# Kernel tuning notes

Measured on AMD Instinct MI355X. Metric: run time of the kernel, lower is better.

## Reference

```python
import jax, jax.numpy as jnp
import numpy as np

B, N, D_MODEL = 4, 4096, 1024
HEADS, DIM_HEAD = 16, 64
HIDDEN = HEADS * DIM_HEAD
SCALE = DIM_HEAD ** -0.5


def setup_inputs() -> dict:
    key = jax.random.key(0)
    k1, k2, k3, k4 = jax.random.split(key, 4)
    x = jax.random.normal(k1, (B, N, D_MODEL), dtype=jnp.float32)
    w_qkv = jax.random.normal(k2, (D_MODEL, 3 * HIDDEN), dtype=jnp.float32) * (D_MODEL ** -0.5)
    w_out = jax.random.normal(k3, (HIDDEN, D_MODEL), dtype=jnp.float32) * (HIDDEN ** -0.5)
    b_out = jax.random.normal(k4, (D_MODEL,), dtype=jnp.float32) * 0.01
    return {"x": x, "w_qkv": w_qkv, "w_out": w_out, "b_out": b_out}


def reference(x, w_qkv, w_out, b_out):
    b, n, _ = x.shape
    qkv = x @ w_qkv  # [b, n, 3*hidden]
    q, k, v = jnp.split(qkv, 3, axis=-1)

    def to_bhdn(t):
        # 'b n (h d) -> b h d n'
        return t.reshape(b, n, HEADS, DIM_HEAD).transpose(0, 2, 3, 1)

    q, k, v = map(to_bhdn, (q, k, v))
    q = jax.nn.softmax(q, axis=-2) * SCALE  # softmax over feature dim d
    k = jax.nn.softmax(k, axis=-1)          # softmax over sequence dim n
    context = jnp.einsum('bhdn,bhen->bhde', k, v)  # [b,h,d,e], d=e=dim_head
    out = jnp.einsum('bhde,bhdn->bhen', context, q)
    # 'b h e n -> b n (h e)'
    out = out.transpose(0, 3, 1, 2).reshape(b, n, HIDDEN)
    return out @ w_out + b_out
```

## Files before the change

kernel.cpp:

```cpp
#include <hip/hip_runtime.h>
#include <hip/hip_bf16.h>


typedef unsigned short u16t;
typedef __bf16 bf16x8 __attribute__((ext_vector_type(8)));
typedef float f32x4 __attribute__((ext_vector_type(4)));
typedef unsigned short ushort8 __attribute__((ext_vector_type(8)));

__device__ __forceinline__ u16t f2bf(float f) {
    union { float f; unsigned int u; } v; v.f = f;
    unsigned int r = v.u + 0x7fffu + ((v.u >> 16) & 1u);
    return (u16t)(r >> 16);
}
__device__ __forceinline__ float bf2f(u16t h) {
    union { unsigned int u; float f; } v; v.u = ((unsigned int)h) << 16;
    return v.f;
}

#define GLOAD_LDS16(gptr, lptr) \
    __builtin_amdgcn_global_load_lds((const __attribute__((address_space(1))) unsigned int*)(gptr), \
                                     (__attribute__((address_space(3))) unsigned int*)(lptr), 16, 0, 0)
#define SFENCE asm volatile("" ::: "memory")

__global__ __launch_bounds__(256) void prep_kernel(const float* __restrict__ x, u16t* __restrict__ xb,
                                                   const float* __restrict__ w_qkv, u16t* __restrict__ wqkvT,
                                                   const float* __restrict__ w_out, u16t* __restrict__ woutT,
                                                   float* __restrict__ zbase) {
    int bid = blockIdx.x, t = threadIdx.x;
    if (bid < 2048) {
        int i = (bid * 256 + t) * 4;
        for (; i < 16777216; i += 2048 * 256 * 4) {
            float4 v = *(const float4*)(x + i);
            ushort4 o;
            o.x = f2bf(v.x); o.y = f2bf(v.y); o.z = f2bf(v.z); o.w = f2bf(v.w);
            *(ushort4*)(xb + i) = o;
        }
        return;
    }
    if (bid >= 6144) {
        float4* z = (float4*)zbase;
        int i = (bid - 6144) * 256 + t;
        for (; i < 69632; i += 68 * 256) z[i] = make_float4(0.f, 0.f, 0.f, 0.f);
        return;
    }
    __shared__ float tile[32][33];
    const float* in; u16t* out; int R, C, bx, by;
    if (bid < 5120) { in = w_qkv; out = wqkvT; R = 1024; C = 3072; int b2 = bid - 2048; bx = b2 % 96; by = b2 / 96; }
    else            { in = w_out; out = woutT; R = 1024; C = 1024; int b3 = bid - 5120; bx = b3 & 31; by = b3 >> 5; }
    int c0 = bx * 32, r0 = by * 32;
    int tx = t & 31, ty = t >> 5;
    for (int i = 0; i < 32; i += 8)
        tile[ty + i][tx] = in[(size_t)(r0 + ty + i) * C + c0 + tx];
    __syncthreads();
    for (int i = 0; i < 32; i += 8)
        out[(size_t)(c0 + ty + i) * R + r0 + tx] = f2bf(tile[tx][ty + i]);
}

template<int OUTF32, int BIAS, int BATCHB, int KSUM>
__device__ __forceinline__ void gemm256_body(const u16t* __restrict__ A, const u16t* __restrict__ Bt,
                                             void* __restrict__ Cout, const float* __restrict__ bias,
                                             float* __restrict__ ksum,
                                             int M, int N, int K, int NBX, int lda) {
    __shared__ __align__(16) u16t lds[65536];
    const int t = threadIdx.x;
    const int l = t & 63, w = t >> 6;
    const int wm = w >> 2, wn = w & 3;

    int cpx = gridDim.x >> 3;
    int wg = ((int)blockIdx.x & 7) * cpx + ((int)blockIdx.x >> 3);
    int bx = wg % NBX, by = wg / NBX;
    const int m0 = by * 256, n0 = bx * 256;
    const int NT = K >> 6;
    if (BATCHB) Bt += (size_t)(by >> 4) << 20;

    const int colk0 = ((l >> 4) ^ (l & 7)) * 8;
    const int colk1 = colk0 ^ 32;
    const int abase = (wm * 32 + (l & 15)) * 64;
    const int bbase = 16384 + (wn >> 1) * 8192 + ((wn & 1) * 64 + (l & 15)) * 64;

    const int rr = w * 8 + (l >> 3);
    const int coloff = ((l ^ (l >> 3)) & 7) * 8;
    const int rowA = rr + ((rr >= 32) ? 96 : 0);
    const u16t* pa_st = A  + (size_t)(m0 + rowA) * lda + coloff;
    const u16t* pb_st = Bt + (size_t)(n0 + rr) * K + coloff;
    const int so = w * 512;

#define SPAIR(qq, kto, pb) do { \
    size_t k64_ = (size_t)(kto) * 64; \
    if ((qq) == 0) { \
        GLOAD_LDS16(pb_st + k64_,                  &lds[(pb) * 32768 + 16384 + so]); \
        GLOAD_LDS16(pb_st + k64_ + (size_t)64 * K, &lds[(pb) * 32768 + 20480 + so]); \
    } else if ((qq) == 1) { \
        GLOAD_LDS16(pb_st + k64_ + (size_t)128 * K, &lds[(pb) * 32768 + 24576 + so]); \
        GLOAD_LDS16(pb_st + k64_ + (size_t)192 * K, &lds[(pb) * 32768 + 28672 + so]); \
    } else if ((qq) == 2) { \
        GLOAD_LDS16(pa_st + k64_,                    &lds[(pb) * 32768 + so]); \
        GLOAD_LDS16(pa_st + k64_ + (size_t)32 * lda, &lds[(pb) * 32768 + 4096 + so]); \
    } else { \
        GLOAD_LDS16(pa_st + k64_ + (size_t)64 * lda, &lds[(pb) * 32768 + 8192 + so]); \
        GLOAD_LDS16(pa_st + k64_ + (size_t)96 * lda, &lds[(pb) * 32768 + 12288 + so]); \
    } \
} while (0)

    f32x4 acc[8][4] = {};

    SPAIR(0, 0, 0); SPAIR(1, 0, 0); SPAIR(2, 0, 0);
    SFENCE;
    SPAIR(3, 0, 0);

    for (int kt = 0; kt < NT; ++kt) {
        const int p = kt & 1;
        const bool sn = (kt + 1 < NT);
        const u16t* lA = &lds[p * 32768];

        asm volatile("s_waitcnt vmcnt(2)" ::: "memory");
        __builtin_amdgcn_s_barrier();

        bf16x8 bfr[4][2];
#pragma unroll
        for (int ni = 0; ni < 4; ++ni) {
            bfr[ni][0] = *(const bf16x8*)&lA[bbase + ni * 1024 + colk0];
            bfr[ni][1] = *(const bf16x8*)&lA[bbase + ni * 1024 + colk1];
        }
        bf16x8 af1[2][2][2];
#pragma unroll
        for (int g = 0; g < 2; ++g) {
            af1[g][0][0] = *(const bf16x8*)&lA[g * 4096 + abase + colk0];
            af1[g][0][1] = *(const bf16x8*)&lA[g * 4096 + abase + colk1];
            af1[g][1][0] = *(const bf16x8*)&lA[g * 4096 + abase + 1024 + colk0];
            af1[g][1][1] = *(const bf16x8*)&lA[g * 4096 + abase + 1024 + colk1];
        }
        if (sn) { SPAIR(0, kt + 1, p ^ 1); SPAIR(1, kt + 1, p ^ 1); SPAIR(2, kt + 1, p ^ 1); }
        __builtin_amdgcn_s_setprio(1);
#pragma unroll
        for (int g = 0; g < 2; ++g)
#pragma unroll
            for (int dm = 0; dm < 2; ++dm)
#pragma unroll
                for (int ni = 0; ni < 4; ++ni)
#pragma unroll
                    for (int kk = 0; kk < 2; ++kk)
                        acc[g * 2 + dm][ni] = __builtin_amdgcn_mfma_f32_16x16x32_bf16(
                            af1[g][dm][kk], bfr[ni][kk], acc[g * 2 + dm][ni], 0, 0, 0);
        __builtin_amdgcn_s_setprio(0);

        if (sn) asm volatile("s_waitcnt vmcnt(6)" ::: "memory");
        else    asm volatile("s_waitcnt vmcnt(0)" ::: "memory");
        __builtin_amdgcn_s_barrier();

        bf16x8 af2[2][2][2];
#pragma unroll
        for (int g = 0; g < 2; ++g) {
            af2[g][0][0] = *(const bf16x8*)&lA[(g + 2) * 4096 + abase + colk0];
            af2[g][0][1] = *(const bf16x8*)&lA[(g + 2) * 4096 + abase + colk1];
            af2[g][1][0] = *(const bf16x8*)&lA[(g + 2) * 4096 + abase + 1024 + colk0];
            af2[g][1][1] = *(const bf16x8*)&lA[(g + 2) * 4096 + abase + 1024 + colk1];
        }
        if (sn) SPAIR(3, kt + 1, p ^ 1);
        __builtin_amdgcn_s_setprio(1);
#pragma unroll
        for (int g = 0; g < 2; ++g)
#pragma unroll
            for (int dm = 0; dm < 2; ++dm)
#pragma unroll
                for (int ni = 0; ni < 4; ++ni)
#pragma unroll
                    for (int kk = 0; kk < 2; ++kk)
                        acc[4 + g * 2 + dm][ni] = __builtin_amdgcn_mfma_f32_16x16x32_bf16(
                            af2[g][dm][kk], bfr[ni][kk], acc[4 + g * 2 + dm][ni], 0, 0, 0);
        __builtin_amdgcn_s_setprio(0);
    }
#undef SPAIR

    if (KSUM && n0 >= 1024 && n0 < 2048) {
#pragma unroll
        for (int ni = 0; ni < 4; ++ni) {
            int col = n0 + wn * 64 + ni * 16 + (l & 15);
            float se = 0.f;
#pragma unroll
            for (int mi = 0; mi < 8; ++mi) {
                int row = m0 + wm * 128 + mi * 16 + ((l >> 4) << 2);
#pragma unroll
                for (int j = 0; j < 4; ++j) {
                    float e = __expf(acc[mi][ni][j]);
                    se += e;
                    ((u16t*)Cout)[(size_t)(row + j) * N + col] = f2bf(e);
                }
            }
            se += __shfl_xor(se, 16);
            se += __shfl_xor(se, 32);
            if ((l >> 4) == 0)
                atomicAdd(&ksum[(by >> 4) * 1024 + (n0 - 1024) + wn * 64 + ni * 16 + l], se);
        }
    } else {
#pragma unroll
        for (int mi = 0; mi < 8; ++mi) {
            int row = m0 + wm * 128 + mi * 16 + ((l >> 4) << 2);
#pragma unroll
            for (int ni = 0; ni < 4; ++ni) {
                int col = n0 + wn * 64 + ni * 16 + (l & 15);
                float bv = BIAS ? bias[col] : 0.f;
#pragma unroll
                for (int j = 0; j < 4; ++j) {
                    float v = acc[mi][ni][j] + bv;
                    if (OUTF32) ((float*)Cout)[(size_t)(row + j) * N + col] = v;
                    else        ((u16t*)Cout)[(size_t)(row + j) * N + col] = f2bf(v);
                }
            }
        }
    }
}

__global__ __launch_bounds__(512, 2) void gemm_qkv(const u16t* __restrict__ A, const u16t* __restrict__ Bt,
                                                   u16t* __restrict__ C, float* __restrict__ ksum) {
    gemm256_body<0, 0, 0, 1>(A, Bt, C, nullptr, ksum, 16384, 3072, 1024, 12, 1024);
}

__global__ __launch_bounds__(512, 2) void gemm_out(const u16t* __restrict__ A, const u16t* __restrict__ Bt,
                                                   float* __restrict__ C, const float* __restrict__ bias) {
    gemm256_body<1, 1, 1, 0>(A, Bt, C, bias, nullptr, 16384, 1024, 1024, 4, 3072);
}

__global__ __launch_bounds__(256) void post_qkv(u16t* __restrict__ qkv,
                                                const float* __restrict__ ksum,
                                                float* __restrict__ ctxT) {
    int bid = blockIdx.x, t = threadIdx.x;
    if (bid < 512) {
        int bh = bid >> 3, chunk = bid & 7;
        int b = bh >> 4, h = bh & 15;
        __shared__ u16t kT[64 * 136];
        __shared__ u16t vT[64 * 136];
        int lane = t & 63, w = t >> 6;
        f32x4 acc[4] = {};
        for (int sub = 0; sub < 4; sub++) {
            size_t rowbase = ((size_t)b * 4096 + chunk * 512 + sub * 128) * 3072 + h * 64;
#pragma unroll
            for (int i = 0; i < 4; i++) {
                int P = t + 256 * i;
                int n = P >> 3, c = P & 7;
                size_t ro = rowbase + (size_t)n * 3072 + c * 8;
                ushort8 k8 = *(const ushort8*)(&qkv[ro + 1024]);
                ushort8 v8 = *(const ushort8*)(&qkv[ro + 2048]);
                int nx = n ^ (c << 3);
#pragma unroll
                for (int j = 0; j < 8; j++) {
                    kT[(c * 8 + j) * 136 + nx] = k8[j];
                    vT[(c * 8 + j) * 136 + nx] = v8[j];
                }
            }
            __syncthreads();
#pragma unroll
            for (int ks = 0; ks < 4; ks++) {
                int er = w * 16 + (lane & 15);
                int nb = ks * 32 + ((lane >> 4) << 3);
                bf16x8 a = *(const bf16x8*)(&vT[er * 136 + (nb ^ ((er >> 3) << 3))]);
#pragma unroll
                for (int ct = 0; ct < 4; ct++) {
                    int dr = ct * 16 + (lane & 15);
                    bf16x8 bb = *(const bf16x8*)(&kT[dr * 136 + (nb ^ ((dr >> 3) << 3))]);
                    acc[ct] = __builtin_amdgcn_mfma_f32_16x16x32_bf16(a, bb, acc[ct], 0, 0, 0);
                }
            }
            __syncthreads();
        }
#pragma unroll
        for (int ct = 0; ct < 4; ct++) {
            int e = w * 16 + ((lane >> 4) << 2);
            int dd = ct * 16 + (lane & 15);
            float gi = 1.0f / ksum[b * 1024 + h * 64 + dd];
#pragma unroll
            for (int j = 0; j < 4; j++)
                atomicAdd(&ctxT[(size_t)bh * 4096 + (e + j) * 64 + dd], acc[ct][j] * gi);
        }
        return;
    }
    int qb = bid - 512;
#pragma unroll
    for (int it = 0; it < 8; ++it) {
        int r = qb * 256 + it * 32 + (t >> 3);
        size_t addr = (size_t)(r >> 4) * 3072 + (r & 15) * 64 + (t & 7) * 8;
        ushort8 ch = *(const ushort8*)(&qkv[addr]);
        float v0 = bf2f(ch[0]), v1 = bf2f(ch[1]), v2 = bf2f(ch[2]), v3 = bf2f(ch[3]);
        float v4 = bf2f(ch[4]), v5 = bf2f(ch[5]), v6 = bf2f(ch[6]), v7 = bf2f(ch[7]);
        float m = fmaxf(fmaxf(fmaxf(v0, v1), fmaxf(v2, v3)), fmaxf(fmaxf(v4, v5), fmaxf(v6, v7)));
        m = fmaxf(m, __shfl_xor(m, 1)); m = fmaxf(m, __shfl_xor(m, 2)); m = fmaxf(m, __shfl_xor(m, 4));
        float e0 = __expf(v0 - m), e1 = __expf(v1 - m), e2 = __expf(v2 - m), e3 = __expf(v3 - m);
        float e4 = __expf(v4 - m), e5 = __expf(v5 - m), e6 = __expf(v6 - m), e7 = __expf(v7 - m);
        float s = e0 + e1 + e2 + e3 + e4 + e5 + e6 + e7;
        s += __shfl_xor(s, 1); s += __shfl_xor(s, 2); s += __shfl_xor(s, 4);
        float inv = 0.125f / s;
        ushort8 o;
        o[0] = f2bf(e0 * inv); o[1] = f2bf(e1 * inv); o[2] = f2bf(e2 * inv); o[3] = f2bf(e3 * inv);
        o[4] = f2bf(e4 * inv); o[5] = f2bf(e5 * inv); o[6] = f2bf(e6 * inv); o[7] = f2bf(e7 * inv);
        *(ushort8*)(&qkv[addr]) = o;
    }
}

__global__ __launch_bounds__(256) void w2_kernel(const float* __restrict__ ctxT,
                                                 const u16t* __restrict__ woutT,
                                                 u16t* __restrict__ w2t) {
    int bh = blockIdx.x, jc = blockIdx.y;
    int b = bh >> 4, h = bh & 15;
    __shared__ u16t cb[64][72];
    __shared__ u16t wl[256][72];
    int t = threadIdx.x;
#pragma unroll
    for (int i = 0; i < 16; i++) {
        int f = t + 256 * i;
        cb[f & 63][f >> 6] = f2bf(ctxT[(size_t)bh * 4096 + f]);
    }
#pragma unroll
    for (int i = 0; i < 8; i++) {
        int f = t + 256 * i;
        int r = f >> 3, q = f & 7;
        *(uint4*)(&wl[r][q * 8]) = *(const uint4*)(&woutT[(size_t)(jc * 256 + r) * 1024 + h * 64 + q * 8]);
    }
    __syncthreads();
    int l = t & 63, w = t >> 6;
    f32x4 acc[4][4] = {};
#pragma unroll
    for (int kk = 0; kk < 2; kk++) {
        bf16x8 af[4], bfr[4];
#pragma unroll
        for (int mt = 0; mt < 4; mt++)
            af[mt] = *(const bf16x8*)&wl[w * 64 + mt * 16 + (l & 15)][(l >> 4) * 8 + kk * 32];
#pragma unroll
        for (int nt = 0; nt < 4; nt++)
            bfr[nt] = *(const bf16x8*)&cb[nt * 16 + (l & 15)][(l >> 4) * 8 + kk * 32];
#pragma unroll
        for (int mt = 0; mt < 4; mt++)
#pragma unroll
            for (int nt = 0; nt < 4; nt++)
                acc[mt][nt] = __builtin_amdgcn_mfma_f32_16x16x32_bf16(af[mt], bfr[nt], acc[mt][nt], 0, 0, 0);
    }
#pragma unroll
    for (int mt = 0; mt < 4; mt++) {
        int j = jc * 256 + w * 64 + mt * 16 + ((l >> 4) << 2);
#pragma unroll
        for (int nt = 0; nt < 4; nt++) {
            int dd = nt * 16 + (l & 15);
#pragma unroll
            for (int jj = 0; jj < 4; jj++)
                w2t[((size_t)b << 20) + (size_t)(j + jj) * 1024 + h * 64 + dd] = f2bf(acc[mt][nt][jj]);
        }
    }
}


extern "C" void kernel_launch(void* const* d_in, const int* in_sizes, int n_in,
                              void* d_out, int out_size, void* d_ws, size_t ws_size,
                              hipStream_t stream) {
    const float* x     = (const float*)d_in[0];
    const float* w_qkv = (const float*)d_in[1];
    const float* w_out = (const float*)d_in[2];
    const float* b_out = (const float*)d_in[3];
    float* out = (float*)d_out;
    char* ws = (char*)d_ws;

    size_t o_xb    = 0;
    size_t o_wqkvT = 33554432;
    size_t o_woutT = 39845888;
    size_t o_qkv   = 41943040;
    size_t o_ctx   = 142606336;
    size_t o_ksum  = 143654912;
    size_t needed  = 143720448;
    if (ws_size < needed) return;

    u16t* xb     = (u16t*)(ws + o_xb);
    u16t* w2t    = (u16t*)(ws + o_xb);
    u16t* wqkvT  = (u16t*)(ws + o_wqkvT);
    u16t* woutT  = (u16t*)(ws + o_woutT);
    u16t* qkvb   = (u16t*)(ws + o_qkv);
    float* ctxT  = (float*)(ws + o_ctx);
    float* ksum  = (float*)(ws + o_ksum);

    prep_kernel<<<6212, 256, 0, stream>>>(x, xb, w_qkv, wqkvT, w_out, woutT, ctxT);

    gemm_qkv<<<768, 512, 0, stream>>>(xb, wqkvT, qkvb, ksum);

    post_qkv<<<1536, 256, 0, stream>>>(qkvb, ksum, ctxT);

    w2_kernel<<<dim3(64, 4), 256, 0, stream>>>(ctxT, woutT, w2t);

    gemm_out<<<256, 512, 0, stream>>>(qkvb, w2t, out, b_out);
}
```

Before: 193.8 us.

## Fuse K-softmax exp and KᵀV context into QKV GEMM epilogue, drop K/V round trip

The QKV GEMM now pairs the K and V columns of a head pair in each output tile. Its epilogue computes exp(K), stages exp(K) and V transposed in LDS, runs a small MFMA KᵀV, and atomically accumulates the context, so K and V are never written to or re-read from global memory. The K-softmax normalisation (1/ksum) moves into w2_kernel, and the Q feature softmax becomes a standalone kernel. The cost is extra LDS work and synchronisation in the GEMM epilogue, plus many more atomics on ctxT, one per 256-row tile instead of per 512-row chunk.

```diff
diff --git a/kernel.cpp b/kernel.cpp
--- a/kernel.cpp
+++ b/kernel.cpp
@@ -6,6 +6,7 @@
 typedef __bf16 bf16x8 __attribute__((ext_vector_type(8)));
 typedef float f32x4 __attribute__((ext_vector_type(4)));
 typedef unsigned short ushort8 __attribute__((ext_vector_type(8)));
+typedef unsigned short u16x4 __attribute__((ext_vector_type(4)));
 
 __device__ __forceinline__ u16t f2bf(float f) {
     union { float f; unsigned int u; } v; v.f = f;
@@ -56,10 +57,10 @@
         out[(size_t)(c0 + ty + i) * R + r0 + tx] = f2bf(tile[tx][ty + i]);
 }
 
-template<int OUTF32, int BIAS, int BATCHB, int KSUM>
+template<int OUTF32, int BIAS, int BATCHB, int KV>
 __device__ __forceinline__ void gemm256_body(const u16t* __restrict__ A, const u16t* __restrict__ Bt,
                                              void* __restrict__ Cout, const float* __restrict__ bias,
-                                             float* __restrict__ ksum,
+                                             float* __restrict__ ksum, float* __restrict__ ctxT,
                                              int M, int N, int K, int NBX, int lda) {
     __shared__ __align__(16) u16t lds[65536];
     const int t = threadIdx.x;
@@ -81,18 +82,22 @@
     const int rr = w * 8 + (l >> 3);
     const int coloff = ((l ^ (l >> 3)) & 7) * 8;
     const int rowA = rr + ((rr >= 32) ? 96 : 0);
-    const u16t* pa_st = A  + (size_t)(m0 + rowA) * lda + coloff;
-    const u16t* pb_st = Bt + (size_t)(n0 + rr) * K + coloff;
+    const u16t* pa_st = A + (size_t)(m0 + rowA) * lda + coloff;
+    int rb0, rb1;
+    if (KV && bx >= 4) { int hp = bx - 4; rb0 = 1024 + hp * 128; rb1 = 2048 + hp * 128; }
+    else               { rb0 = n0; rb1 = n0 + 128; }
+    const u16t* pb0 = Bt + (size_t)(rb0 + rr) * K + coloff;
+    const u16t* pb1 = Bt + (size_t)(rb1 + rr) * K + coloff;
     const int so = w * 512;
 
 #define SPAIR(qq, kto, pb) do { \
     size_t k64_ = (size_t)(kto) * 64; \
     if ((qq) == 0) { \
-        GLOAD_LDS16(pb_st + k64_,                  &lds[(pb) * 32768 + 16384 + so]); \
-        GLOAD_LDS16(pb_st + k64_ + (size_t)64 * K, &lds[(pb) * 32768 + 20480 + so]); \
+        GLOAD_LDS16(pb0 + k64_,                  &lds[(pb) * 32768 + 16384 + so]); \
+        GLOAD_LDS16(pb0 + k64_ + (size_t)64 * K, &lds[(pb) * 32768 + 20480 + so]); \
     } else if ((qq) == 1) { \
-        GLOAD_LDS16(pb_st + k64_ + (size_t)128 * K, &lds[(pb) * 32768 + 24576 + so]); \
-        GLOAD_LDS16(pb_st + k64_ + (size_t)192 * K, &lds[(pb) * 32768 + 28672 + so]); \
+        GLOAD_LDS16(pb1 + k64_,                  &lds[(pb) * 32768 + 24576 + so]); \
+        GLOAD_LDS16(pb1 + k64_ + (size_t)64 * K, &lds[(pb) * 32768 + 28672 + so]); \
     } else if ((qq) == 2) { \
         GLOAD_LDS16(pa_st + k64_,                    &lds[(pb) * 32768 + so]); \
         GLOAD_LDS16(pa_st + k64_ + (size_t)32 * lda, &lds[(pb) * 32768 + 4096 + so]); \
@@ -172,25 +177,75 @@
     }
 #undef SPAIR
 
-    if (KSUM && n0 >= 1024 && n0 < 2048) {
-#pragma unroll
-        for (int ni = 0; ni < 4; ++ni) {
-            int col = n0 + wn * 64 + ni * 16 + (l & 15);
-            float se = 0.f;
-#pragma unroll
-            for (int mi = 0; mi < 8; ++mi) {
-                int row = m0 + wm * 128 + mi * 16 + ((l >> 4) << 2);
-#pragma unroll
-                for (int j = 0; j < 4; ++j) {
-                    float e = __expf(acc[mi][ni][j]);
-                    se += e;
-                    ((u16t*)Cout)[(size_t)(row + j) * N + col] = f2bf(e);
+    if (KV && bx >= 4) {
+        const int hp = bx - 4;
+        const int bb = by >> 4;
+        __syncthreads();
+        u16t* ekT = lds;
+        u16t* vT  = lds + 32768;
+#define EADDR(dp, r) ((dp) * 256 + ((r) ^ (((dp) & 15) << 2)))
+        if (wn < 2) {
+#pragma unroll
+            for (int ni = 0; ni < 4; ++ni) {
+                int dp = wn * 64 + ni * 16 + (l & 15);
+                float se = 0.f;
+#pragma unroll
+                for (int mi = 0; mi < 8; ++mi) {
+                    int r0 = wm * 128 + mi * 16 + ((l >> 4) << 2);
+                    u16x4 pk;
+#pragma unroll
+                    for (int j = 0; j < 4; ++j) { float e = __expf(acc[mi][ni][j]); se += e; pk[j] = f2bf(e); }
+                    *(u16x4*)&ekT[EADDR(dp, r0)] = pk;
+                }
+                se += __shfl_xor(se, 16);
+                se += __shfl_xor(se, 32);
+                if ((l >> 4) == 0)
+                    atomicAdd(&ksum[bb * 1024 + hp * 128 + dp], se);
+            }
+        } else {
+#pragma unroll
+            for (int ni = 0; ni < 4; ++ni) {
+                int ep = (wn - 2) * 64 + ni * 16 + (l & 15);
+#pragma unroll
+                for (int mi = 0; mi < 8; ++mi) {
+                    int r0 = wm * 128 + mi * 16 + ((l >> 4) << 2);
+                    u16x4 pv;
+#pragma unroll
+                    for (int j = 0; j < 4; ++j) pv[j] = f2bf(acc[mi][ni][j]);
+                    *(u16x4*)&vT[EADDR(ep, r0)] = pv;
                 }
             }
-            se += __shfl_xor(se, 16);
-            se += __shfl_xor(se, 32);
-            if ((l >> 4) == 0)
-                atomicAdd(&ksum[(by >> 4) * 1024 + (n0 - 1024) + wn * 64 + ni * 16 + l], se);
+        }
+        __syncthreads();
+        const int head = w >> 2, tn = w & 3;
+        const int dp2 = head * 64 + tn * 16 + (l & 15);
+        const int sb2 = (dp2 & 15) << 2;
+        f32x4 acc2[4] = {};
+#pragma unroll
+        for (int ks = 0; ks < 8; ++ks) {
+            int rk = ks * 32 + ((l >> 4) << 3);
+            union { u16x4 h[2]; bf16x8 v; } bu;
+            bu.h[0] = *(const u16x4*)&ekT[dp2 * 256 + (rk ^ sb2)];
+            bu.h[1] = *(const u16x4*)&ekT[dp2 * 256 + ((rk + 4) ^ sb2)];
+#pragma unroll
+            for (int tm = 0; tm < 4; ++tm) {
+                int ep = head * 64 + tm * 16 + (l & 15);
+                int sa = (ep & 15) << 2;
+                union { u16x4 h[2]; bf16x8 v; } au;
+                au.h[0] = *(const u16x4*)&vT[ep * 256 + (rk ^ sa)];
+                au.h[1] = *(const u16x4*)&vT[ep * 256 + ((rk + 4) ^ sa)];
+                acc2[tm] = __builtin_amdgcn_mfma_f32_16x16x32_bf16(au.v, bu.v, acc2[tm], 0, 0, 0);
+            }
+        }
+#undef EADDR
+        int bh = bb * 16 + hp * 2 + head;
+#pragma unroll
+        for (int tm = 0; tm < 4; ++tm) {
+            int e = tm * 16 + ((l >> 4) << 2);
+            int dd = tn * 16 + (l & 15);
+#pragma unroll
+            for (int j = 0; j < 4; ++j)
+                atomicAdd(&ctxT[(size_t)bh * 4096 + (e + j) * 64 + dd], acc2[tm][j]);
         }
     } else {
 #pragma unroll
@@ -212,72 +267,21 @@
 }
 
 __global__ __launch_bounds__(512, 2) void gemm_qkv(const u16t* __restrict__ A, const u16t* __restrict__ Bt,
-                                                   u16t* __restrict__ C, float* __restrict__ ksum) {
-    gemm256_body<0, 0, 0, 1>(A, Bt, C, nullptr, ksum, 16384, 3072, 1024, 12, 1024);
+                                                   u16t* __restrict__ C, float* __restrict__ ksum,
+                                                   float* __restrict__ ctxT) {
+    gemm256_body<0, 0, 0, 1>(A, Bt, C, nullptr, ksum, ctxT, 16384, 3072, 1024, 12, 1024);
 }
 
 __global__ __launch_bounds__(512, 2) void gemm_out(const u16t* __restrict__ A, const u16t* __restrict__ Bt,
                                                    float* __restrict__ C, const float* __restrict__ bias) {
-    gemm256_body<1, 1, 1, 0>(A, Bt, C, bias, nullptr, 16384, 1024, 1024, 4, 3072);
-}
-
-__global__ __launch_bounds__(256) void post_qkv(u16t* __restrict__ qkv,
-                                                const float* __restrict__ ksum,
-                                                float* __restrict__ ctxT) {
-    int bid = blockIdx.x, t = threadIdx.x;
-    if (bid < 512) {
-        int bh = bid >> 3, chunk = bid & 7;
-        int b = bh >> 4, h = bh & 15;
-        __shared__ u16t kT[64 * 136];
-        __shared__ u16t vT[64 * 136];
-        int lane = t & 63, w = t >> 6;
-        f32x4 acc[4] = {};
-        for (int sub = 0; sub < 4; sub++) {
-            size_t rowbase = ((size_t)b * 4096 + chunk * 512 + sub * 128) * 3072 + h * 64;
-#pragma unroll
-            for (int i = 0; i < 4; i++) {
-                int P = t + 256 * i;
-                int n = P >> 3, c = P & 7;
-                size_t ro = rowbase + (size_t)n * 3072 + c * 8;
-                ushort8 k8 = *(const ushort8*)(&qkv[ro + 1024]);
-                ushort8 v8 = *(const ushort8*)(&qkv[ro + 2048]);
-                int nx = n ^ (c << 3);
-#pragma unroll
-                for (int j = 0; j < 8; j++) {
-                    kT[(c * 8 + j) * 136 + nx] = k8[j];
-                    vT[(c * 8 + j) * 136 + nx] = v8[j];
-                }
-            }
-            __syncthreads();
-#pragma unroll
-            for (int ks = 0; ks < 4; ks++) {
-                int er = w * 16 + (lane & 15);
-                int nb = ks * 32 + ((lane >> 4) << 3);
-                bf16x8 a = *(const bf16x8*)(&vT[er * 136 + (nb ^ ((er >> 3) << 3))]);
-#pragma unroll
-                for (int ct = 0; ct < 4; ct++) {
-                    int dr = ct * 16 + (lane & 15);
-                    bf16x8 bb = *(const bf16x8*)(&kT[dr * 136 + (nb ^ ((dr >> 3) << 3))]);
-                    acc[ct] = __builtin_amdgcn_mfma_f32_16x16x32_bf16(a, bb, acc[ct], 0, 0, 0);
-                }
-            }
-            __syncthreads();
-        }
-#pragma unroll
-        for (int ct = 0; ct < 4; ct++) {
-            int e = w * 16 + ((lane >> 4) << 2);
-            int dd = ct * 16 + (lane & 15);
-            float gi = 1.0f / ksum[b * 1024 + h * 64 + dd];
-#pragma unroll
-            for (int j = 0; j < 4; j++)
-                atomicAdd(&ctxT[(size_t)bh * 4096 + (e + j) * 64 + dd], acc[ct][j] * gi);
-        }
-        return;
-    }
-    int qb = bid - 512;
+    gemm256_body<1, 1, 1, 0>(A, Bt, C, bias, nullptr, nullptr, 16384, 1024, 1024, 4, 3072);
+}
+
+__global__ __launch_bounds__(256) void q_softmax_rows(u16t* __restrict__ qkv) {
+    int t = threadIdx.x;
 #pragma unroll
     for (int it = 0; it < 8; ++it) {
-        int r = qb * 256 + it * 32 + (t >> 3);
+        int r = blockIdx.x * 256 + it * 32 + (t >> 3);
         size_t addr = (size_t)(r >> 4) * 3072 + (r & 15) * 64 + (t & 7) * 8;
         ushort8 ch = *(const ushort8*)(&qkv[addr]);
         float v0 = bf2f(ch[0]), v1 = bf2f(ch[1]), v2 = bf2f(ch[2]), v3 = bf2f(ch[3]);
@@ -297,6 +301,7 @@
 }
 
 __global__ __launch_bounds__(256) void w2_kernel(const float* __restrict__ ctxT,
+                                                 const float* __restrict__ ksum,
                                                  const u16t* __restrict__ woutT,
                                                  u16t* __restrict__ w2t) {
     int bh = blockIdx.x, jc = blockIdx.y;
@@ -304,10 +309,11 @@
     __shared__ u16t cb[64][72];
     __shared__ u16t wl[256][72];
     int t = threadIdx.x;
+    float ginv = 1.0f / ksum[b * 1024 + h * 64 + (t & 63)];
 #pragma unroll
     for (int i = 0; i < 16; i++) {
         int f = t + 256 * i;
-        cb[f & 63][f >> 6] = f2bf(ctxT[(size_t)bh * 4096 + f]);
+        cb[f & 63][f >> 6] = f2bf(ctxT[(size_t)bh * 4096 + f] * ginv);
     }
 #pragma unroll
     for (int i = 0; i < 8; i++) {
@@ -376,11 +382,11 @@
 
     prep_kernel<<<6212, 256, 0, stream>>>(x, xb, w_qkv, wqkvT, w_out, woutT, ctxT);
 
-    gemm_qkv<<<768, 512, 0, stream>>>(xb, wqkvT, qkvb, ksum);
-
-    post_qkv<<<1536, 256, 0, stream>>>(qkvb, ksum, ctxT);
-
-    w2_kernel<<<dim3(64, 4), 256, 0, stream>>>(ctxT, woutT, w2t);
+    gemm_qkv<<<768, 512, 0, stream>>>(xb, wqkvT, qkvb, ksum, ctxT);
+
+    w2_kernel<<<dim3(64, 4), 256, 0, stream>>>(ctxT, ksum, woutT, w2t);
+
+    q_softmax_rows<<<1024, 256, 0, stream>>>(qkvb);
 
     gemm_out<<<256, 512, 0, stream>>>(qkvb, w2t, out, b_out);
 }
```

After: 174.1 us, median of 2. -10.2%, faster.
